# Performance work log

Hardware: AMD Instinct MI355X
Metric: run time of the kernel (lower is better)

Reference implementation:

```python
import jax, jax.numpy as jnp
import numpy as np

B, TZ, TU = 32, 16, 128
E, H, V = 512, 1024, 32000
FREQ_THRES = 4   # cfg.freq_thres: zero out copy prob for most-frequent tokens
LN_EPS = 1e-3


def setup_inputs() -> dict:
    key = jax.random.key(0)
    ks = jax.random.split(key, 16)
    s = lambda k, shape, sc=0.02: jax.random.normal(k, shape, jnp.float32) * sc
    return dict(
        z_enc_out=jax.random.normal(ks[0], (TZ, B, H), jnp.float32),
        pz_proba=jax.nn.softmax(jax.random.normal(ks[1], (TZ, B, V), jnp.float32), axis=-1),
        u_enc_out=jax.random.normal(ks[2], (TU, B, H), jnp.float32),
        m_t_input=jax.random.randint(ks[3], (1, B), 0, V),
        last_hidden=jax.random.normal(ks[4], (1, B, H), jnp.float32),
        emb=s(ks[5], (V, E), 1.0 / np.sqrt(E)),
        Wa_z=s(ks[6], (2 * H, H)), ba_z=jnp.zeros((H,), jnp.float32), v_z=s(ks[7], (H,), 1.0 / np.sqrt(H)),
        Wa_u=s(ks[8], (2 * H, H)), ba_u=jnp.zeros((H,), jnp.float32), v_u=s(ks[9], (H,), 1.0 / np.sqrt(H)),
        W_ih=s(ks[10], (3 * H, E + 2 * H)), W_hh=s(ks[11], (3 * H, H)),
        b_ih=jnp.zeros((3 * H,), jnp.float32), b_hh=jnp.zeros((3 * H,), jnp.float32),
        ln_a=jnp.ones((H,), jnp.float32), ln_b=jnp.zeros((H,), jnp.float32),
        W_proj=s(ks[12], (H, V)), b_proj=jnp.zeros((V,), jnp.float32),
        W_c=s(ks[13], (2 * H, H)), b_c=jnp.zeros((H,), jnp.float32),
        W_v1=s(ks[14], (H, 1)), b_v1=jnp.zeros((1,), jnp.float32),
    )


def _attn(hidden, enc, Wa, ba, v):
    # hidden [1,B,H], enc [T,B,H] -> context [1,B,H]
    hh = jnp.broadcast_to(hidden, enc.shape)                       # [T,B,H]
    energy = jnp.tanh(jnp.concatenate([hh, enc], -1) @ Wa + ba)    # [T,B,H]
    scores = jnp.einsum('tbh,h->bt', energy, v)                    # [B,T]
    w = jax.nn.softmax(scores, axis=1)
    return jnp.einsum('bt,tbh->bh', w, enc)[None]                  # [1,B,H]


def _layernorm(x, a, b):
    mu = jnp.mean(x, axis=-1, keepdims=True)
    sigma = jnp.std(x, axis=-1, keepdims=True, ddof=1)  # torch.std is unbiased
    return (x - mu) / (sigma + LN_EPS) * a + b


def reference(z_enc_out, pz_proba, u_enc_out, m_t_input, last_hidden,
              emb, Wa_z, ba_z, v_z, Wa_u, ba_u, v_u,
              W_ih, W_hh, b_ih, b_hh, ln_a, ln_b,
              W_proj, b_proj, W_c, b_c, W_v1, b_v1):
    m_embed = emb[m_t_input]                                       # [1,B,E]
    z_ctx = _attn(last_hidden, z_enc_out, Wa_z, ba_z, v_z)         # [1,B,H]
    u_ctx = _attn(last_hidden, u_enc_out, Wa_u, ba_u, v_u)         # [1,B,H]
    x = jnp.concatenate([z_ctx, u_ctx, m_embed], -1)[0]            # [B,2H+E]
    h = last_hidden[0]                                             # [B,H]
    # single-step GRU (torch gate order: r, z, n)
    gi = x @ W_ih.T + b_ih
    gh = h @ W_hh.T + b_hh
    ir, iz, inn = jnp.split(gi, 3, axis=-1)
    hr, hz, hn = jnp.split(gh, 3, axis=-1)
    r = jax.nn.sigmoid(ir + hr)
    zg = jax.nn.sigmoid(iz + hz)
    n = jnp.tanh(inn + r * hn)
    h_new = (1.0 - zg) * n + zg * h                                # [B,H]
    gru_out = _layernorm(h_new, ln_a, ln_b)                        # [B,H]
    gen_score = gru_out @ W_proj + b_proj                          # [B,V]
    # tanh-linear copy score over z positions
    g_rep = jnp.broadcast_to(gru_out[None], z_enc_out.shape)       # [Tz,B,H]
    zc = jnp.tanh(jnp.concatenate([z_enc_out, g_rep], -1) @ W_c + b_c)  # [Tz,B,H]
    zc = (zc @ W_v1 + b_v1)[..., 0].T                              # [B,Tz]
    # joint softmax over [gen | copy]
    scores = jax.nn.softmax(jnp.concatenate([gen_score, zc], axis=1), axis=1)
    gen_p, copy_p = scores[:, :V], scores[:, V:]
    copy_v = jnp.einsum('bt,tbv->bv', copy_p, pz_proba)            # mask_prob bmm
    freq_mask = (jnp.arange(V) >= FREQ_THRES).astype(gen_p.dtype)
    proba = gen_p + copy_v * freq_mask
    return proba, h_new[None]
```

## Files before the change

kernel.cpp:

```cpp
#include <hip/hip_runtime.h>
#include <stdint.h>

#define B_ 32
#define TZ_ 16
#define TU_ 128
#define E_ 512
#define H_ 1024
#define V_ 32000
#define X_ 2560
#define H3_ 3072
#define LN_EPS_ 0.001f

typedef unsigned short ushort_t;
typedef ushort_t us4 __attribute__((ext_vector_type(4)));
typedef ushort_t us8 __attribute__((ext_vector_type(8)));
typedef short bf16x8 __attribute__((ext_vector_type(8)));
typedef float f32x4 __attribute__((ext_vector_type(4)));

__device__ __forceinline__ float bf2f(ushort_t u){
  union { unsigned int i; float f; } x; x.i = ((unsigned int)u) << 16; return x.f;
}
__device__ __forceinline__ ushort_t f2b(float f){
  union { float f; unsigned int i; } u; u.f = f;
  unsigned int x = u.i;
  return (ushort_t)((x + 0x7fffu + ((x >> 16) & 1u)) >> 16);
}
__device__ __forceinline__ bool is_bf(const void* lnA){
  return *(const unsigned int*)lnA == 0x3F803F80u;
}
__device__ __forceinline__ float ldg_(const void* p, size_t i, bool isb){
  return isb ? bf2f(((const ushort_t*)p)[i]) : ((const float*)p)[i];
}
__device__ __forceinline__ float sigm(float x){ return 1.0f/(1.0f + __expf(-x)); }
__device__ __forceinline__ float tanh_f(float x){
  float cx = fminf(fmaxf(x, -9.0f), 9.0f);
  float t = __expf(2.0f*cx);
  return (t - 1.0f)/(t + 1.0f);
}

__global__ void k0_init(const void* lh, const void* emb, const int* mt,
                        const void* ba_z, const void* ba_u, const void* b_c,
                        const void* b_ih, const void* b_hh, const void* bpj,
                        const void* lnA,
                        ushort_t* hb, ushort_t* xb, float* hWaZ, float* hWaU,
                        float* sz, float* su, float* gruWc, float* gi, float* gh,
                        float* genscore){
  bool isb = is_bf(lnA);
  int i = blockIdx.x*256 + threadIdx.x;
  if (i < 32768){ hb[i] = f2b(ldg_(lh, i, isb)); return; }
  i -= 32768;
  if (i < 16384){ int b = i >> 9, e = i & 511;
    xb[b*X_ + 2048 + e] = f2b(ldg_(emb, (size_t)(unsigned)mt[b]*E_ + e, isb)); return; }
  i -= 16384;
  if (i < 32768){ hWaZ[i] = ldg_(ba_z, i & 1023, isb); return; }
  i -= 32768;
  if (i < 32768){ hWaU[i] = ldg_(ba_u, i & 1023, isb); return; }
  i -= 32768;
  if (i < 4608){ if (i < 512) sz[i] = 0.f; else su[i-512] = 0.f; return; }
  i -= 4608;
  if (i < 32768){ gruWc[i] = ldg_(b_c, i & 1023, isb); return; }
  i -= 32768;
  if (i < 98304){ gi[i] = ldg_(b_ih, i % H3_, isb); return; }
  i -= 98304;
  if (i < 98304){ gh[i] = ldg_(b_hh, i % H3_, isb); return; }
  i -= 98304;
  if (i < 1024000){
    int b = i / V_;
    int v = i - b*V_;
    genscore[(size_t)b*V_ + v] = ldg_(bpj, v, isb);
  }
}

__global__ void kC_cvt(const void* uenc, const void* zenc, const void* Wih, const void* Whh,
                       const void* lnA,
                       ushort_t* uB, ushort_t* zB, ushort_t* WihB, ushort_t* WhhB){
  bool isb = is_bf(lnA);
  long long i = (long long)(blockIdx.x*256 + threadIdx.x) * 8;
  const long long NU = (long long)TU_*B_*H_;
  const long long NZ = (long long)TZ_*B_*H_;
  const long long NI = (long long)H3_*X_;
  const long long NH = (long long)H3_*H_;
  const void* src; ushort_t* dst;
  if (i < NU){ src = uenc; dst = uB; }
  else if ((i -= NU) < NZ){ src = zenc; dst = zB; }
  else if ((i -= NZ) < NI){ src = Wih; dst = WihB; }
  else if ((i -= NI) < NH){ src = Whh; dst = WhhB; }
  else return;
  if (isb){
    *(us8*)&dst[i] = *(const us8*)((const ushort_t*)src + i);
  } else {
    const float* s = (const float*)src + i;
    float4 a0 = *(const float4*)s, a1 = *(const float4*)(s + 4);
    us8 o;
    o[0]=f2b(a0.x); o[1]=f2b(a0.y); o[2]=f2b(a0.z); o[3]=f2b(a0.w);
    o[4]=f2b(a1.x); o[5]=f2b(a1.y); o[6]=f2b(a1.z); o[7]=f2b(a1.w);
    *(us8*)&dst[i] = o;
  }
}

__global__ void kT_transpose(const void* Wz, const void* Wu, const void* Wc, const void* lnA,
                             ushort_t* tZ, ushort_t* tU, ushort_t* tC,
                             ushort_t* tZt, ushort_t* tUt, ushort_t* tCb){
  bool isb = is_bf(lnA);
  int w = blockIdx.z;
  const void* src = (w==0||w==3)? Wz : (w==1||w==4)? Wu : Wc;
  size_t base = (w==0||w==1||w==5) ? (size_t)H_*H_ : 0;
  ushort_t* dst = (w==0)? tZ : (w==1)? tU : (w==2)? tC : (w==3)? tZt : (w==4)? tUt : tCb;
  __shared__ ushort_t T[64][68];
  int k0 = blockIdx.x*64, j0 = blockIdx.y*64;
  int tx = threadIdx.x & 15, ty = threadIdx.x >> 4;
  if (isb){
    const ushort_t* s = (const ushort_t*)src + base;
    #pragma unroll
    for (int rr=0; rr<4; ++rr){
      int row = ty + rr*16;
      *(us4*)&T[row][tx*4] = *(const us4*)&s[(size_t)(k0+row)*H_ + j0 + tx*4];
    }
  } else {
    const float* s = (const float*)src + base;
    #pragma unroll
    for (int rr=0; rr<4; ++rr){
      int row = ty + rr*16;
      #pragma unroll
      for (int c=0;c<4;c++)
        T[row][tx*4+c] = f2b(s[(size_t)(k0+row)*H_ + j0 + tx*4 + c]);
    }
  }
  __syncthreads();
  #pragma unroll
  for (int rr=0; rr<4; ++rr){
    int row = ty + rr*16;
    us4 o;
    o[0]=T[tx*4+0][row]; o[1]=T[tx*4+1][row]; o[2]=T[tx*4+2][row]; o[3]=T[tx*4+3][row];
    *(us4*)&dst[(size_t)(j0+row)*H_ + k0 + tx*4] = o;
  }
}

__global__ __launch_bounds__(256) void kg_mfma(const ushort_t* Ab0, const ushort_t* Ab1,
                                               const ushort_t* W0, const ushort_t* W1,
                                               float* out0, float* out1, int N){
  const ushort_t* Ab = blockIdx.z ? Ab1 : Ab0;
  const ushort_t* WT = blockIdx.z ? W1 : W0;
  float* out = blockIdx.z ? out1 : out0;
  int j0 = blockIdx.x*128;
  int kchunk = H_ / gridDim.y;
  int kb = blockIdx.y*kchunk;
  __shared__ ushort_t Bs[128*32];
  int tid = threadIdx.x, wid = tid >> 6, lane = tid & 63;
  int q = lane >> 4, n = lane & 15;
  int rrow = tid >> 2, t4 = tid & 3;
  f32x4 acc[2][2];
  #pragma unroll
  for (int r=0;r<2;r++)
    #pragma unroll
    for (int c=0;c<2;c++)
      #pragma unroll
      for (int e=0;e<4;e++) acc[r][c][e] = 0.f;

  for (int kt = 0; kt < kchunk; kt += 32){
    int k = kb + kt;
    __syncthreads();
    #pragma unroll
    for (int p=0;p<2;p++){
      const ushort_t* srcB = WT + (size_t)(j0 + p*64 + rrow)*H_ + k + t4*8;
      __builtin_amdgcn_global_load_lds(srcB, &Bs[(p*64 + wid*16)*32], 16, 0, 0);
    }
    __syncthreads();
    bf16x8 af[2], bfr[2];
    #pragma unroll
    for (int r=0;r<2;r++) af[r] = *(const bf16x8*)&Ab[(size_t)(r*16 + n)*H_ + k + q*8];
    #pragma unroll
    for (int c=0;c<2;c++) bfr[c] = *(const bf16x8*)&Bs[(wid*32 + c*16 + n)*32 + q*8];
    #pragma unroll
    for (int r=0;r<2;r++)
      #pragma unroll
      for (int c=0;c<2;c++)
        acc[r][c] = __builtin_amdgcn_mfma_f32_16x16x32_bf16(af[r], bfr[c], acc[r][c], 0, 0, 0);
  }
  #pragma unroll
  for (int r=0;r<2;r++)
    #pragma unroll
    for (int c=0;c<2;c++)
      #pragma unroll
      for (int i=0;i<4;i++){
        int b = r*16 + q*4 + i;
        int j = j0 + wid*32 + c*16 + n;
        unsafeAtomicAdd(&out[(size_t)b*N + j], acc[r][c][i]);
      }
}

__global__ __launch_bounds__(256) void k2_mfma(const ushort_t* Ab, const ushort_t* WB,
                                               float* out, int K, int kchunk){
  int j0 = blockIdx.x*128;
  int kb = blockIdx.y*kchunk;
  __shared__ ushort_t Bs[128*32];
  int tid = threadIdx.x, wid = tid >> 6, lane = tid & 63;
  int q = lane >> 4, n = lane & 15;
  int rrow = tid >> 2, t4 = tid & 3;
  f32x4 acc[2][2];
  #pragma unroll
  for (int r=0;r<2;r++)
    #pragma unroll
    for (int c=0;c<2;c++)
      #pragma unroll
      for (int e=0;e<4;e++) acc[r][c][e] = 0.f;

  for (int kt = 0; kt < kchunk; kt += 32){
    int k = kb + kt;
    __syncthreads();
    #pragma unroll
    for (int p=0;p<2;p++){
      const ushort_t* srcB = WB + (size_t)(j0 + p*64 + rrow)*K + k + t4*8;
      __builtin_amdgcn_global_load_lds(srcB, &Bs[(p*64 + wid*16)*32], 16, 0, 0);
    }
    __syncthreads();
    bf16x8 af[2], bfr[2];
    #pragma unroll
    for (int r=0;r<2;r++) af[r] = *(const bf16x8*)&Ab[(size_t)(r*16 + n)*K + k + q*8];
    #pragma unroll
    for (int c=0;c<2;c++) bfr[c] = *(const bf16x8*)&Bs[(wid*32 + c*16 + n)*32 + q*8];
    #pragma unroll
    for (int r=0;r<2;r++)
      #pragma unroll
      for (int c=0;c<2;c++)
        acc[r][c] = __builtin_amdgcn_mfma_f32_16x16x32_bf16(af[r], bfr[c], acc[r][c], 0, 0, 0);
  }
  #pragma unroll
  for (int r=0;r<2;r++)
    #pragma unroll
    for (int c=0;c<2;c++)
      #pragma unroll
      for (int i=0;i<4;i++){
        int b = r*16 + q*4 + i;
        int j = j0 + wid*32 + c*16 + n;
        unsafeAtomicAdd(&out[(size_t)b*H3_ + j], acc[r][c][i]);
      }
}

__global__ __launch_bounds__(256) void k6p_mfma(const ushort_t* grub, const void* Wp,
                                                const void* lnA, float* genscore){
  bool isb = is_bf(lnA);
  int j0 = blockIdx.x*128;
  int kb = blockIdx.y*256;
  __shared__ float Ts[32][129];
  int tid = threadIdx.x, wid = tid >> 6, lane = tid & 63;
  int q = lane >> 4, n = lane & 15;
  int lrow = tid >> 3, lcol = (tid & 7)*16;
  f32x4 acc[2][2];
  #pragma unroll
  for (int r=0;r<2;r++)
    #pragma unroll
    for (int c=0;c<2;c++)
      #pragma unroll
      for (int e=0;e<4;e++) acc[r][c][e] = 0.f;

  for (int kt = 0; kt < 256; kt += 32){
    int k = kb + kt;
    __syncthreads();
    if (isb){
      const ushort_t* s = (const ushort_t*)Wp + (size_t)(k + lrow)*V_ + j0 + lcol;
      us8 a0 = *(const us8*)s;
      us8 a1 = *(const us8*)(s + 8);
      #pragma unroll
      for (int e=0;e<8;e++){ Ts[lrow][lcol+e] = bf2f(a0[e]); Ts[lrow][lcol+8+e] = bf2f(a1[e]); }
    } else {
      const float* s = (const float*)Wp + (size_t)(k + lrow)*V_ + j0 + lcol;
      float4 f0 = *(const float4*)s,     f1 = *(const float4*)(s+4);
      float4 f2 = *(const float4*)(s+8), f3 = *(const float4*)(s+12);
      *(float4*)&Ts[lrow][lcol]    = f0;
      *(float4*)&Ts[lrow][lcol+4]  = f1;
      *(float4*)&Ts[lrow][lcol+8]  = f2;
      *(float4*)&Ts[lrow][lcol+12] = f3;
    }
    __syncthreads();
    bf16x8 af[2], bfr[2];
    #pragma unroll
    for (int r=0;r<2;r++) af[r] = *(const bf16x8*)&grub[(size_t)(r*16 + n)*H_ + k + q*8];
    #pragma unroll
    for (int c=0;c<2;c++){
      int vl = wid*32 + c*16 + n;
      us8 o;
      #pragma unroll
      for (int e=0;e<8;e++) o[e] = f2b(Ts[q*8 + e][vl]);
      bfr[c] = *(bf16x8*)&o;
    }
    #pragma unroll
    for (int r=0;r<2;r++)
      #pragma unroll
      for (int c=0;c<2;c++)
        acc[r][c] = __builtin_amdgcn_mfma_f32_16x16x32_bf16(af[r], bfr[c], acc[r][c], 0, 0, 0);
  }
  #pragma unroll
  for (int r=0;r<2;r++)
    #pragma unroll
    for (int c=0;c<2;c++)
      #pragma unroll
      for (int i=0;i<4;i++){
        int b = r*16 + q*4 + i;
        int v = j0 + wid*32 + c*16 + n;
        unsafeAtomicAdd(&genscore[(size_t)b*V_ + v], acc[r][c][i]);
      }
}

__global__ __launch_bounds__(256) void k3_mfma(
    const ushort_t* uB, const ushort_t* zB,
    const ushort_t* tU, const ushort_t* tZ, const ushort_t* tC,
    const float* hWaU, const float* hWaZ,
    const void* v_u, const void* v_z, const void* lnA,
    float* su, float* sz, float* zcpre)
{
  bool isb = is_bf(lnA);
  int which = blockIdx.z;
  int bx = blockIdx.x, nt = blockIdx.y;
  int mt;
  const ushort_t* A; const ushort_t* BT;
  if (which == 0){ A = uB; BT = tU; mt = bx; }
  else {
    int lo = (which==1) ? 8 : 12;
    if (bx < lo || bx >= lo+4) return;
    mt = bx - lo;
    A = zB; BT = (which==1) ? tZ : tC;
  }
  __shared__ ushort_t As[128*32];
  __shared__ ushort_t Bs[64*32];
  int tid = threadIdx.x;
  int wid = tid >> 6, lane = tid & 63;
  int q = lane >> 4, n = lane & 15;
  int wm = wid & 1, wn = wid >> 1;
  int r0 = mt*128, j0 = nt*64;
  f32x4 acc[4][2];
  #pragma unroll
  for (int a=0;a<4;a++)
    #pragma unroll
    for (int c=0;c<2;c++)
      #pragma unroll
      for (int e=0;e<4;e++) acc[a][c][e] = 0.f;

  int rrow = tid >> 2, t4 = tid & 3;

  for (int kt = 0; kt < 32; ++kt){
    __syncthreads();
    #pragma unroll
    for (int p=0;p<2;p++){
      const ushort_t* srcA = A + (size_t)(r0 + p*64 + rrow)*H_ + kt*32 + t4*8;
      __builtin_amdgcn_global_load_lds(srcA, &As[(p*64 + wid*16)*32], 16, 0, 0);
    }
    {
      const ushort_t* srcB = BT + (size_t)(j0 + rrow)*H_ + kt*32 + t4*8;
      __builtin_amdgcn_global_load_lds(srcB, &Bs[(wid*16)*32], 16, 0, 0);
    }
    __syncthreads();
    bf16x8 af[4], bfr[2];
    #pragma unroll
    for (int f=0;f<4;f++) af[f] = *(const bf16x8*)&As[(wm*64 + f*16 + n)*32 + q*8];
    #pragma unroll
    for (int f=0;f<2;f++) bfr[f] = *(const bf16x8*)&Bs[(wn*32 + f*16 + n)*32 + q*8];
    #pragma unroll
    for (int fr=0;fr<4;fr++)
      #pragma unroll
      for (int fn=0;fn<2;fn++)
        acc[fr][fn] = __builtin_amdgcn_mfma_f32_16x16x32_bf16(af[fr], bfr[fn], acc[fr][fn], 0, 0, 0);
  }

  if (which < 2){
    const float* pre = (which==0) ? hWaU : hWaZ;
    const void* vv = (which==0) ? v_u : v_z;
    float* score = (which==0) ? su : sz;
    float s[4][4];
    #pragma unroll
    for (int fr=0;fr<4;fr++)
      #pragma unroll
      for (int i=0;i<4;i++) s[fr][i]=0.f;
    #pragma unroll
    for (int fr=0;fr<4;fr++){
      #pragma unroll
      for (int fn=0;fn<2;fn++){
        int j  = j0 + wn*32 + fn*16 + n;
        float vj = ldg_(vv, j, isb);
        #pragma unroll
        for (int i=0;i<4;i++){
          int rl = wm*64 + fr*16 + q*4 + i;
          int b  = rl & 31;
          s[fr][i] += tanh_f(acc[fr][fn][i] + pre[b*H_ + j]) * vj;
        }
      }
    }
    #pragma unroll
    for (int fr=0;fr<4;fr++)
      #pragma unroll
      for (int i=0;i<4;i++){
        float t = s[fr][i];
        t += __shfl_xor(t, 1);
        t += __shfl_xor(t, 2);
        t += __shfl_xor(t, 4);
        t += __shfl_xor(t, 8);
        if (n == 0){
          int rl = wm*64 + fr*16 + q*4 + i;
          unsafeAtomicAdd(&score[r0 + rl], t);
        }
      }
  } else {
    #pragma unroll
    for (int fr=0;fr<4;fr++)
      #pragma unroll
      for (int fn=0;fn<2;fn++)
        #pragma unroll
        for (int i=0;i<4;i++){
          int rl = wm*64 + fr*16 + q*4 + i;
          int jl = wn*32 + fn*16 + n;
          zcpre[(size_t)(r0 + rl)*H_ + j0 + jl] = acc[fr][fn][i];
        }
  }
}

__global__ void k4_ctx(const float* sz, const float* su,
                       const void* zenc, const void* uenc, const void* lnA, ushort_t* xb){
  bool isb = is_bf(lnA);
  int jc = blockIdx.x, b = blockIdx.y, which = blockIdx.z;
  int T = which ? TU_ : TZ_;
  const float* sc = which ? su : sz;
  const void* enc = which ? uenc : zenc;
  __shared__ float red[256];
  __shared__ float w[TU_];
  int tid = threadIdx.x;
  float v = (tid < T) ? sc[tid*B_ + b] : -1e30f;
  red[tid] = v; __syncthreads();
  for (int s=128; s>0; s>>=1){ if (tid < s) red[tid] = fmaxf(red[tid], red[tid+s]); __syncthreads(); }
  float m = red[0]; __syncthreads();
  float e = (tid < T) ? __expf(v - m) : 0.f;
  red[tid] = e; __syncthreads();
  for (int s=128; s>0; s>>=1){ if (tid < s) red[tid] += red[tid+s]; __syncthreads(); }
  float S = red[0]; __syncthreads();
  if (tid < T) w[tid] = e / S;
  __syncthreads();
  int j = jc*256 + tid;
  float acc = 0.f;
  #pragma unroll 4
  for (int t=0; t<T; ++t) acc = fmaf(w[t], ldg_(enc, (size_t)(t*B_ + b)*H_ + j, isb), acc);
  xb[b*X_ + which*H_ + j] = f2b(acc);
}

__global__ __launch_bounds__(1024) void k5_gru(const float* gi, const float* gh,
                       const void* lh, const void* ln_a, const void* ln_b,
                       ushort_t* grub, float* hout){
  bool isb = is_bf(ln_a);
  int b = blockIdx.x, tid = threadIdx.x;
  __shared__ float red[1024];
  int j = tid;
  float ir = gi[(size_t)b*H3_ + j], iz = gi[(size_t)b*H3_ + 1024 + j], inn = gi[(size_t)b*H3_ + 2048 + j];
  float hr = gh[(size_t)b*H3_ + j], hz = gh[(size_t)b*H3_ + 1024 + j], hn = gh[(size_t)b*H3_ + 2048 + j];
  float hv = ldg_(lh, b*H_ + j, isb);
  float r  = sigm(ir + hr);
  float zg = sigm(iz + hz);
  float nn = tanh_f(inn + r*hn);
  float h2 = (1.f - zg)*nn + zg*hv;
  hout[b*H_ + j] = h2;
  red[tid] = h2; __syncthreads();
  for (int s=512;s>0;s>>=1){ if(tid<s) red[tid]+=red[tid+s]; __syncthreads(); }
  float mu = red[0] / 1024.f; __syncthreads();
  red[tid] = h2*h2; __syncthreads();
  for (int s=512;s>0;s>>=1){ if(tid<s) red[tid]+=red[tid+s]; __syncthreads(); }
  float var = (red[0] - 1024.f*mu*mu) / 1023.f;
  float sg = sqrtf(fmaxf(var, 0.f));
  float inv = 1.f/(sg + LN_EPS_);
  float g = (h2 - mu)*inv*ldg_(ln_a, j, isb) + ldg_(ln_b, j, isb);
  grub[b*H_ + j] = f2b(g);
}

__global__ void k7_zc(const float* zcpre, const float* gruWc, const void* Wv1,
                      const void* b_v1, const void* lnA, float* zc){
  bool isb = is_bf(lnA);
  int r = blockIdx.x, b = r & 31, tid = threadIdx.x;
  __shared__ float red[256];
  float s = 0.f;
  #pragma unroll
  for (int jj=0;jj<4;jj++){
    int j = tid + jj*256;
    float e = tanh_f(zcpre[(size_t)r*H_ + j] + gruWc[b*H_ + j]);
    s = fmaf(e, ldg_(Wv1, j, isb), s);
  }
  red[tid] = s; __syncthreads();
  for (int st=128;st>0;st>>=1){ if(tid<st) red[tid]+=red[tid+st]; __syncthreads(); }
  if (tid==0) zc[r] = red[0] + ldg_(b_v1, 0, isb);
}

__global__ void k8a(const float* genscore, float* statpart){
  int v = blockIdx.x*256 + threadIdx.x;
  int b = blockIdx.y, tid = threadIdx.x;
  __shared__ float red[256];
  float g = genscore[(size_t)b*V_ + v];
  red[tid] = g; __syncthreads();
  for (int s=128;s>0;s>>=1){ if(tid<s) red[tid]=fmaxf(red[tid],red[tid+s]); __syncthreads(); }
  float m = red[0]; __syncthreads();
  float e = __expf(g - m);
  red[tid] = e; __syncthreads();
  for (int s=128;s>0;s>>=1){ if(tid<s) red[tid]+=red[tid+s]; __syncthreads(); }
  if (tid==0){ statpart[(b*125 + blockIdx.x)*2] = m; statpart[(b*125 + blockIdx.x)*2+1] = red[0]; }
}

__global__ void k8b(const float* statpart, const float* zc, float* stats, float* copyp){
  int b = blockIdx.x, tid = threadIdx.x;
  __shared__ float red[128];
  float m = -1e30f, s = 0.f;
  if (tid < 125){ m = statpart[(b*125 + tid)*2]; s = statpart[(b*125 + tid)*2 + 1]; }
  float zv = (tid < 16) ? zc[tid*B_ + b] : -1e30f;
  red[tid] = fmaxf(m, zv); __syncthreads();
  for (int st=64;st>0;st>>=1){ if(tid<st) red[tid]=fmaxf(red[tid],red[tid+st]); __syncthreads(); }
  float M = red[0]; __syncthreads();
  float zp = (tid < 125) ? s*__expf(m - M) : 0.f;
  if (tid < 16) zp += __expf(zv - M);
  red[tid] = zp; __syncthreads();
  for (int st=64;st>0;st>>=1){ if(tid<st) red[tid]+=red[tid+st]; __syncthreads(); }
  float invZ = 1.f/red[0];
  if (tid < 16) copyp[b*16 + tid] = __expf(zv - M)*invZ;
  if (tid == 0){ stats[b*2] = M; stats[b*2+1] = invZ; }
}

__global__ void k8c(const float* genscore, const float* stats, const float* copyp,
                    const void* pz, const void* lnA, float* out){
  bool isb = is_bf(lnA);
  int v = blockIdx.x*256 + threadIdx.x;
  int b = blockIdx.y;
  float M = stats[b*2], invZ = stats[b*2+1];
  float p = __expf(genscore[(size_t)b*V_ + v] - M)*invZ;
  if (v >= 4){
    float cv = 0.f;
    if (isb){
      const ushort_t* pzp = (const ushort_t*)pz;
      #pragma unroll
      for (int t=0;t<16;t++)
        cv = fmaf(copyp[b*16 + t], bf2f(pzp[(size_t)(t*B_ + b)*V_ + v]), cv);
    } else {
      const float* pzp = (const float*)pz;
      #pragma unroll
      for (int t=0;t<16;t++)
        cv = fmaf(copyp[b*16 + t], pzp[(size_t)(t*B_ + b)*V_ + v], cv);
    }
    p += cv;
  }
  out[(size_t)b*V_ + v] = p;
}

extern "C" void kernel_launch(void* const* d_in, const int* in_sizes, int n_in,
                              void* d_out, int out_size, void* d_ws, size_t ws_size,
                              hipStream_t stream){
  const void* z_enc = d_in[0];
  const void* pz    = d_in[1];
  const void* u_enc = d_in[2];
  const int*  m_t   = (const int*)d_in[3];
  const void* lh    = d_in[4];
  const void* emb   = d_in[5];
  const void* Wa_z  = d_in[6];
  const void* ba_z  = d_in[7];
  const void* v_z   = d_in[8];
  const void* Wa_u  = d_in[9];
  const void* ba_u  = d_in[10];
  const void* v_u   = d_in[11];
  const void* W_ih  = d_in[12];
  const void* W_hh  = d_in[13];
  const void* b_ih  = d_in[14];
  const void* b_hh  = d_in[15];
  const void* ln_a  = d_in[16];
  const void* ln_b  = d_in[17];
  const void* W_proj= d_in[18];
  const void* b_proj= d_in[19];
  const void* W_c   = d_in[20];
  const void* b_c   = d_in[21];
  const void* W_v1  = d_in[22];
  const void* b_v1  = d_in[23];

  float* wsf = (float*)d_ws;
  size_t o = 0;
  auto alloc = [&](size_t n){ float* p = wsf + o; o += n; return p; };
  float* hWaZ  = alloc(B_*H_);
  float* hWaU  = alloc(B_*H_);
  float* sz    = alloc(TZ_*B_);
  float* su    = alloc(TU_*B_);
  float* gruWc = alloc(B_*H_);
  float* zcpre = alloc((size_t)TZ_*B_*H_);
  float* zcv   = alloc(TZ_*B_);
  float* gi    = alloc((size_t)B_*H3_);
  float* gh    = alloc((size_t)B_*H3_);
  float* genscore = alloc((size_t)B_*V_);
  float* statpart = alloc(B_*125*2);
  float* stats = alloc(B_*2);
  float* copyp = alloc(B_*TZ_);
  o = (o + 7) & ~(size_t)7;
  ushort_t* wT = (ushort_t*)(wsf + o);
  ushort_t* tZ  = wT;
  ushort_t* tU  = wT + (size_t)H_*H_;
  ushort_t* tC  = wT + (size_t)2*H_*H_;
  ushort_t* tZt = wT + (size_t)3*H_*H_;
  ushort_t* tUt = wT + (size_t)4*H_*H_;
  ushort_t* tCb = wT + (size_t)5*H_*H_;
  o += (size_t)6*H_*H_/2;
  ushort_t* uB = (ushort_t*)(wsf + o);
  o += (size_t)TU_*B_*H_/2;
  ushort_t* zB = (ushort_t*)(wsf + o);
  o += (size_t)TZ_*B_*H_/2;
  ushort_t* WihB = (ushort_t*)(wsf + o);
  o += (size_t)H3_*X_/2;
  ushort_t* WhhB = (ushort_t*)(wsf + o);
  o += (size_t)H3_*H_/2;
  ushort_t* xb = (ushort_t*)(wsf + o);
  o += (size_t)B_*X_/2;
  ushort_t* hb = (ushort_t*)(wsf + o);
  o += (size_t)B_*H_/2;
  ushort_t* grub = (ushort_t*)(wsf + o);
  o += (size_t)B_*H_/2;
  float* outp = (float*)d_out;
  float* hout = outp + (size_t)B_*V_;

  k0_init<<<5362, 256, 0, stream>>>(lh, emb, m_t, ba_z, ba_u, b_c, b_ih, b_hh, b_proj, ln_a,
                                    hb, xb, hWaZ, hWaU, sz, su, gruWc, gi, gh, genscore);
  kC_cvt<<<7680, 256, 0, stream>>>(u_enc, z_enc, W_ih, W_hh, ln_a, uB, zB, WihB, WhhB);
  kT_transpose<<<dim3(16,16,6), 256, 0, stream>>>(Wa_z, Wa_u, W_c, ln_a, tZ, tU, tC, tZt, tUt, tCb);
  kg_mfma<<<dim3(8,8,2), 256, 0, stream>>>(hb, hb, tZt, tUt, hWaZ, hWaU, H_);
  k2_mfma<<<dim3(24,16), 256, 0, stream>>>(hb, WhhB, gh, H_, 64);
  k3_mfma<<<dim3(32,16,3), 256, 0, stream>>>(uB, zB, tU, tZ, tC, hWaU, hWaZ, v_u, v_z, ln_a, su, sz, zcpre);
  k4_ctx<<<dim3(4,32,2), 256, 0, stream>>>(sz, su, z_enc, u_enc, ln_a, xb);
  k2_mfma<<<dim3(24,20), 256, 0, stream>>>(xb, WihB, gi, X_, 128);
  k5_gru<<<32, 1024, 0, stream>>>(gi, gh, lh, ln_a, ln_b, grub, hout);
  kg_mfma<<<dim3(8,8,1), 256, 0, stream>>>(grub, grub, tCb, tCb, gruWc, gruWc, H_);
  k7_zc<<<512, 256, 0, stream>>>(zcpre, gruWc, W_v1, b_v1, ln_a, zcv);
  k6p_mfma<<<dim3(250,4), 256, 0, stream>>>(grub, W_proj, ln_a, genscore);
  k8a<<<dim3(125,32), 256, 0, stream>>>(genscore, statpart);
  k8b<<<32, 128, 0, stream>>>(statpart, zcv, stats, copyp);
  k8c<<<dim3(125,32), 256, 0, stream>>>(genscore, stats, copyp, pz, ln_a, outp);
}
```

Before: 460.9 us.

## Fuse prep kernels, split-K attention GEMM with separate score kernel

Merges the init, conversion and transpose kernels into one launch that also zeroes the new split-K accumulators. The attention energy GEMM is now split along K into two slices that accumulate atomically into fp32 buffers, and a separate kernel applies tanh and the v projection to produce the scores. The vocab projection also gets twice the K-split. The aim is more blocks in flight and fewer launches. In exchange it writes and re-reads large fp32 energy tensors, needs extra zeroing, and issues more atomics.

```diff
diff --git a/kernel.cpp b/kernel.cpp
--- a/kernel.cpp
+++ b/kernel.cpp
@@ -38,101 +38,114 @@
   return (t - 1.0f)/(t + 1.0f);
 }
 
-__global__ void k0_init(const void* lh, const void* emb, const int* mt,
-                        const void* ba_z, const void* ba_u, const void* b_c,
-                        const void* b_ih, const void* b_hh, const void* bpj,
-                        const void* lnA,
-                        ushort_t* hb, ushort_t* xb, float* hWaZ, float* hWaU,
-                        float* sz, float* su, float* gruWc, float* gi, float* gh,
-                        float* genscore){
+#define PB0 5344
+#define PB1 13024
+#define PB2 14560
+#define PB3 19680
+__global__ void kprep(const void* lh, const void* emb, const int* mt,
+                      const void* ba_z, const void* ba_u, const void* b_c,
+                      const void* b_ih, const void* b_hh, const void* bpj,
+                      const void* uenc, const void* zenc, const void* Wih, const void* Whh,
+                      const void* Wz, const void* Wu, const void* Wc,
+                      const void* lnA,
+                      ushort_t* hb, ushort_t* xb, float* hWaZ, float* hWaU,
+                      float* gruWc, float* gi, float* gh, float* genscore,
+                      ushort_t* uB, ushort_t* zB, ushort_t* WihB, ushort_t* WhhB,
+                      ushort_t* tZ, ushort_t* tU, ushort_t* tC,
+                      ushort_t* tZt, ushort_t* tUt, ushort_t* tCb,
+                      float* zeroBase){
+  __shared__ ushort_t T[64][68];
   bool isb = is_bf(lnA);
-  int i = blockIdx.x*256 + threadIdx.x;
-  if (i < 32768){ hb[i] = f2b(ldg_(lh, i, isb)); return; }
-  i -= 32768;
-  if (i < 16384){ int b = i >> 9, e = i & 511;
-    xb[b*X_ + 2048 + e] = f2b(ldg_(emb, (size_t)(unsigned)mt[b]*E_ + e, isb)); return; }
-  i -= 16384;
-  if (i < 32768){ hWaZ[i] = ldg_(ba_z, i & 1023, isb); return; }
-  i -= 32768;
-  if (i < 32768){ hWaU[i] = ldg_(ba_u, i & 1023, isb); return; }
-  i -= 32768;
-  if (i < 4608){ if (i < 512) sz[i] = 0.f; else su[i-512] = 0.f; return; }
-  i -= 4608;
-  if (i < 32768){ gruWc[i] = ldg_(b_c, i & 1023, isb); return; }
-  i -= 32768;
-  if (i < 98304){ gi[i] = ldg_(b_ih, i % H3_, isb); return; }
-  i -= 98304;
-  if (i < 98304){ gh[i] = ldg_(b_hh, i % H3_, isb); return; }
-  i -= 98304;
-  if (i < 1024000){
-    int b = i / V_;
-    int v = i - b*V_;
-    genscore[(size_t)b*V_ + v] = ldg_(bpj, v, isb);
-  }
-}
-
-__global__ void kC_cvt(const void* uenc, const void* zenc, const void* Wih, const void* Whh,
-                       const void* lnA,
-                       ushort_t* uB, ushort_t* zB, ushort_t* WihB, ushort_t* WhhB){
-  bool isb = is_bf(lnA);
-  long long i = (long long)(blockIdx.x*256 + threadIdx.x) * 8;
-  const long long NU = (long long)TU_*B_*H_;
-  const long long NZ = (long long)TZ_*B_*H_;
-  const long long NI = (long long)H3_*X_;
-  const long long NH = (long long)H3_*H_;
-  const void* src; ushort_t* dst;
-  if (i < NU){ src = uenc; dst = uB; }
-  else if ((i -= NU) < NZ){ src = zenc; dst = zB; }
-  else if ((i -= NZ) < NI){ src = Wih; dst = WihB; }
-  else if ((i -= NI) < NH){ src = Whh; dst = WhhB; }
-  else return;
-  if (isb){
-    *(us8*)&dst[i] = *(const us8*)((const ushort_t*)src + i);
-  } else {
-    const float* s = (const float*)src + i;
-    float4 a0 = *(const float4*)s, a1 = *(const float4*)(s + 4);
-    us8 o;
-    o[0]=f2b(a0.x); o[1]=f2b(a0.y); o[2]=f2b(a0.z); o[3]=f2b(a0.w);
-    o[4]=f2b(a1.x); o[5]=f2b(a1.y); o[6]=f2b(a1.z); o[7]=f2b(a1.w);
-    *(us8*)&dst[i] = o;
-  }
-}
-
-__global__ void kT_transpose(const void* Wz, const void* Wu, const void* Wc, const void* lnA,
-                             ushort_t* tZ, ushort_t* tU, ushort_t* tC,
-                             ushort_t* tZt, ushort_t* tUt, ushort_t* tCb){
-  bool isb = is_bf(lnA);
-  int w = blockIdx.z;
-  const void* src = (w==0||w==3)? Wz : (w==1||w==4)? Wu : Wc;
-  size_t base = (w==0||w==1||w==5) ? (size_t)H_*H_ : 0;
-  ushort_t* dst = (w==0)? tZ : (w==1)? tU : (w==2)? tC : (w==3)? tZt : (w==4)? tUt : tCb;
-  __shared__ ushort_t T[64][68];
-  int k0 = blockIdx.x*64, j0 = blockIdx.y*64;
-  int tx = threadIdx.x & 15, ty = threadIdx.x >> 4;
-  if (isb){
-    const ushort_t* s = (const ushort_t*)src + base;
+  int bid = blockIdx.x, tid = threadIdx.x;
+  if (bid < PB0){
+    int i = bid*256 + tid;
+    if (i < 32768){ hb[i] = f2b(ldg_(lh, i, isb)); return; }
+    i -= 32768;
+    if (i < 16384){ int b = i >> 9, e = i & 511;
+      xb[b*X_ + 2048 + e] = f2b(ldg_(emb, (size_t)(unsigned)mt[b]*E_ + e, isb)); return; }
+    i -= 16384;
+    if (i < 32768){ hWaZ[i] = ldg_(ba_z, i & 1023, isb); return; }
+    i -= 32768;
+    if (i < 32768){ hWaU[i] = ldg_(ba_u, i & 1023, isb); return; }
+    i -= 32768;
+    if (i < 32768){ gruWc[i] = ldg_(b_c, i & 1023, isb); return; }
+    i -= 32768;
+    if (i < 98304){ gi[i] = ldg_(b_ih, i % H3_, isb); return; }
+    i -= 98304;
+    if (i < 98304){ gh[i] = ldg_(b_hh, i % H3_, isb); return; }
+    i -= 98304;
+    if (i < 1024000){
+      int b = i / V_;
+      int v = i - b*V_;
+      genscore[(size_t)b*V_ + v] = ldg_(bpj, v, isb);
+    }
+    return;
+  }
+  if (bid < PB1){
+    long long i = (long long)((bid - PB0)*256 + tid) * 8;
+    const long long NU = (long long)TU_*B_*H_;
+    const long long NZ = (long long)TZ_*B_*H_;
+    const long long NI = (long long)H3_*X_;
+    const long long NH = (long long)H3_*H_;
+    const void* src; ushort_t* dst;
+    if (i < NU){ src = uenc; dst = uB; }
+    else if ((i -= NU) < NZ){ src = zenc; dst = zB; }
+    else if ((i -= NZ) < NI){ src = Wih; dst = WihB; }
+    else if ((i -= NI) < NH){ src = Whh; dst = WhhB; }
+    else return;
+    if (isb){
+      *(us8*)&dst[i] = *(const us8*)((const ushort_t*)src + i);
+    } else {
+      const float* s = (const float*)src + i;
+      float4 a0 = *(const float4*)s, a1 = *(const float4*)(s + 4);
+      us8 o;
+      o[0]=f2b(a0.x); o[1]=f2b(a0.y); o[2]=f2b(a0.z); o[3]=f2b(a0.w);
+      o[4]=f2b(a1.x); o[5]=f2b(a1.y); o[6]=f2b(a1.z); o[7]=f2b(a1.w);
+      *(us8*)&dst[i] = o;
+    }
+    return;
+  }
+  if (bid < PB2){
+    int idx = bid - PB1;
+    int w = idx >> 8;
+    int rem = idx & 255;
+    int bx = rem & 15, by = rem >> 4;
+    const void* src = (w==0||w==3)? Wz : (w==1||w==4)? Wu : Wc;
+    size_t base = (w==0||w==1||w==5) ? (size_t)H_*H_ : 0;
+    ushort_t* dst = (w==0)? tZ : (w==1)? tU : (w==2)? tC : (w==3)? tZt : (w==4)? tUt : tCb;
+    int k0 = bx*64, j0 = by*64;
+    int tx = tid & 15, ty = tid >> 4;
+    if (isb){
+      const ushort_t* s = (const ushort_t*)src + base;
+      #pragma unroll
+      for (int rr=0; rr<4; ++rr){
+        int row = ty + rr*16;
+        *(us4*)&T[row][tx*4] = *(const us4*)&s[(size_t)(k0+row)*H_ + j0 + tx*4];
+      }
+    } else {
+      const float* s = (const float*)src + base;
+      #pragma unroll
+      for (int rr=0; rr<4; ++rr){
+        int row = ty + rr*16;
+        #pragma unroll
+        for (int c=0;c<4;c++)
+          T[row][tx*4+c] = f2b(s[(size_t)(k0+row)*H_ + j0 + tx*4 + c]);
+      }
+    }
+    __syncthreads();
     #pragma unroll
     for (int rr=0; rr<4; ++rr){
       int row = ty + rr*16;
-      *(us4*)&T[row][tx*4] = *(const us4*)&s[(size_t)(k0+row)*H_ + j0 + tx*4];
-    }
-  } else {
-    const float* s = (const float*)src + base;
-    #pragma unroll
-    for (int rr=0; rr<4; ++rr){
-      int row = ty + rr*16;
-      #pragma unroll
-      for (int c=0;c<4;c++)
-        T[row][tx*4+c] = f2b(s[(size_t)(k0+row)*H_ + j0 + tx*4 + c]);
-    }
-  }
-  __syncthreads();
-  #pragma unroll
-  for (int rr=0; rr<4; ++rr){
-    int row = ty + rr*16;
-    us4 o;
-    o[0]=T[tx*4+0][row]; o[1]=T[tx*4+1][row]; o[2]=T[tx*4+2][row]; o[3]=T[tx*4+3][row];
-    *(us4*)&dst[(size_t)(j0+row)*H_ + k0 + tx*4] = o;
+      us4 o;
+      o[0]=T[tx*4+0][row]; o[1]=T[tx*4+1][row]; o[2]=T[tx*4+2][row]; o[3]=T[tx*4+3][row];
+      *(us4*)&dst[(size_t)(j0+row)*H_ + k0 + tx*4] = o;
+    }
+    return;
+  }
+  if (bid < PB3){
+    int i = (bid - PB2)*256 + tid;
+    float4 z = {0.f,0.f,0.f,0.f};
+    *(float4*)&zeroBase[(size_t)i*4] = z;
   }
 }
 
@@ -237,11 +250,100 @@
       }
 }
 
+__global__ __launch_bounds__(256) void kg3_mfma(
+    const ushort_t* uB, const ushort_t* zB,
+    const ushort_t* tU, const ushort_t* tZ, const ushort_t* tC,
+    float* E_u, float* E_z, float* E_c)
+{
+  int bx = blockIdx.x, nt = blockIdx.y, ks = blockIdx.z;
+  int mt;
+  const ushort_t* A; const ushort_t* BT; float* E;
+  if (bx < 32){ A = uB; BT = tU; E = E_u; mt = bx; }
+  else if (bx < 36){ A = zB; BT = tZ; E = E_z; mt = bx - 32; }
+  else { A = zB; BT = tC; E = E_c; mt = bx - 36; }
+  __shared__ ushort_t As[128*32];
+  __shared__ ushort_t Bs[64*32];
+  int tid = threadIdx.x;
+  int wid = tid >> 6, lane = tid & 63;
+  int q = lane >> 4, n = lane & 15;
+  int wm = wid & 1, wn = wid >> 1;
+  int r0 = mt*128, j0 = nt*64;
+  int kbase = ks*512;
+  f32x4 acc[4][2];
+  #pragma unroll
+  for (int a=0;a<4;a++)
+    #pragma unroll
+    for (int c=0;c<2;c++)
+      #pragma unroll
+      for (int e=0;e<4;e++) acc[a][c][e] = 0.f;
+
+  int rrow = tid >> 2, t4 = tid & 3;
+
+  for (int kt = 0; kt < 16; ++kt){
+    int k = kbase + kt*32;
+    __syncthreads();
+    #pragma unroll
+    for (int p=0;p<2;p++){
+      const ushort_t* srcA = A + (size_t)(r0 + p*64 + rrow)*H_ + k + t4*8;
+      __builtin_amdgcn_global_load_lds(srcA, &As[(p*64 + wid*16)*32], 16, 0, 0);
+    }
+    {
+      const ushort_t* srcB = BT + (size_t)(j0 + rrow)*H_ + k + t4*8;
+      __builtin_amdgcn_global_load_lds(srcB, &Bs[(wid*16)*32], 16, 0, 0);
+    }
+    __syncthreads();
+    bf16x8 af[4], bfr[2];
+    #pragma unroll
+    for (int f=0;f<4;f++) af[f] = *(const bf16x8*)&As[(wm*64 + f*16 + n)*32 + q*8];
+    #pragma unroll
+    for (int f=0;f<2;f++) bfr[f] = *(const bf16x8*)&Bs[(wn*32 + f*16 + n)*32 + q*8];
+    #pragma unroll
+    for (int fr=0;fr<4;fr++)
+      #pragma unroll
+      for (int fn=0;fn<2;fn++)
+        acc[fr][fn] = __builtin_amdgcn_mfma_f32_16x16x32_bf16(af[fr], bfr[fn], acc[fr][fn], 0, 0, 0);
+  }
+
+  #pragma unroll
+  for (int fr=0;fr<4;fr++)
+    #pragma unroll
+    for (int fn=0;fn<2;fn++)
+      #pragma unroll
+      for (int i=0;i<4;i++){
+        int rl = wm*64 + fr*16 + q*4 + i;
+        int jl = wn*32 + fn*16 + n;
+        unsafeAtomicAdd(&E[(size_t)(r0 + rl)*H_ + j0 + jl], acc[fr][fn][i]);
+      }
+}
+
+__global__ void kE_score(const float* E_u, const float* E_z,
+                         const float* hWaU, const float* hWaZ,
+                         const void* v_u, const void* v_z, const void* lnA,
+                         float* su, float* sz){
+  bool isb = is_bf(lnA);
+  int r = blockIdx.x, tid = threadIdx.x;
+  const float* E; const float* pre; const void* vv; float* sc; int rr;
+  if (r < 4096){ E = E_u; pre = hWaU; vv = v_u; sc = su; rr = r; }
+  else { E = E_z; pre = hWaZ; vv = v_z; sc = sz; rr = r - 4096; }
+  int b = rr & 31;
+  __shared__ float red[256];
+  float s = 0.f;
+  #pragma unroll
+  for (int jj=0;jj<4;jj++){
+    int j = tid + jj*256;
+    s = fmaf(tanh_f(E[(size_t)rr*H_ + j] + pre[b*H_ + j]), ldg_(vv, j, isb), s);
+  }
+  red[tid] = s; __syncthreads();
+  for (int st=128;st>0;st>>=1){ if(tid<st) red[tid]+=red[tid+st]; __syncthreads(); }
+  if (tid==0) sc[rr] = red[0];
+}
+
 __global__ __launch_bounds__(256) void k6p_mfma(const ushort_t* grub, const void* Wp,
                                                 const void* lnA, float* genscore){
   bool isb = is_bf(lnA);
   int j0 = blockIdx.x*128;
-  int kb = blockIdx.y*256;
+  int kchunk = H_ / gridDim.y;
+  int kb = blockIdx.y*kchunk;
   __shared__ float Ts[32][129];
   int tid = threadIdx.x, wid = tid >> 6, lane = tid & 63;
   int q = lane >> 4, n = lane & 15;
@@ -254,7 +356,7 @@
       #pragma unroll
       for (int e=0;e<4;e++) acc[r][c][e] = 0.f;
 
-  for (int kt = 0; kt < 256; kt += 32){
+  for (int kt = 0; kt < kchunk; kt += 32){
     int k = kb + kt;
     __syncthreads();
     if (isb){
@@ -300,117 +402,6 @@
         int v = j0 + wid*32 + c*16 + n;
         unsafeAtomicAdd(&genscore[(size_t)b*V_ + v], acc[r][c][i]);
       }
-}
-
-__global__ __launch_bounds__(256) void k3_mfma(
-    const ushort_t* uB, const ushort_t* zB,
-    const ushort_t* tU, const ushort_t* tZ, const ushort_t* tC,
-    const float* hWaU, const float* hWaZ,
-    const void* v_u, const void* v_z, const void* lnA,
-    float* su, float* sz, float* zcpre)
-{
-  bool isb = is_bf(lnA);
-  int which = blockIdx.z;
-  int bx = blockIdx.x, nt = blockIdx.y;
-  int mt;
-  const ushort_t* A; const ushort_t* BT;
-  if (which == 0){ A = uB; BT = tU; mt = bx; }
-  else {
-    int lo = (which==1) ? 8 : 12;
-    if (bx < lo || bx >= lo+4) return;
-    mt = bx - lo;
-    A = zB; BT = (which==1) ? tZ : tC;
-  }
-  __shared__ ushort_t As[128*32];
-  __shared__ ushort_t Bs[64*32];
-  int tid = threadIdx.x;
-  int wid = tid >> 6, lane = tid & 63;
-  int q = lane >> 4, n = lane & 15;
-  int wm = wid & 1, wn = wid >> 1;
-  int r0 = mt*128, j0 = nt*64;
-  f32x4 acc[4][2];
-  #pragma unroll
-  for (int a=0;a<4;a++)
-    #pragma unroll
-    for (int c=0;c<2;c++)
-      #pragma unroll
-      for (int e=0;e<4;e++) acc[a][c][e] = 0.f;
-
-  int rrow = tid >> 2, t4 = tid & 3;
-
-  for (int kt = 0; kt < 32; ++kt){
-    __syncthreads();
-    #pragma unroll
-    for (int p=0;p<2;p++){
-      const ushort_t* srcA = A + (size_t)(r0 + p*64 + rrow)*H_ + kt*32 + t4*8;
-      __builtin_amdgcn_global_load_lds(srcA, &As[(p*64 + wid*16)*32], 16, 0, 0);
-    }
-    {
-      const ushort_t* srcB = BT + (size_t)(j0 + rrow)*H_ + kt*32 + t4*8;
-      __builtin_amdgcn_global_load_lds(srcB, &Bs[(wid*16)*32], 16, 0, 0);
-    }
-    __syncthreads();
-    bf16x8 af[4], bfr[2];
-    #pragma unroll
-    for (int f=0;f<4;f++) af[f] = *(const bf16x8*)&As[(wm*64 + f*16 + n)*32 + q*8];
-    #pragma unroll
-    for (int f=0;f<2;f++) bfr[f] = *(const bf16x8*)&Bs[(wn*32 + f*16 + n)*32 + q*8];
-    #pragma unroll
-    for (int fr=0;fr<4;fr++)
-      #pragma unroll
-      for (int fn=0;fn<2;fn++)
-        acc[fr][fn] = __builtin_amdgcn_mfma_f32_16x16x32_bf16(af[fr], bfr[fn], acc[fr][fn], 0, 0, 0);
-  }
-
-  if (which < 2){
-    const float* pre = (which==0) ? hWaU : hWaZ;
-    const void* vv = (which==0) ? v_u : v_z;
-    float* score = (which==0) ? su : sz;
-    float s[4][4];
-    #pragma unroll
-    for (int fr=0;fr<4;fr++)
-      #pragma unroll
-      for (int i=0;i<4;i++) s[fr][i]=0.f;
-    #pragma unroll
-    for (int fr=0;fr<4;fr++){
-      #pragma unroll
-      for (int fn=0;fn<2;fn++){
-        int j  = j0 + wn*32 + fn*16 + n;
-        float vj = ldg_(vv, j, isb);
-        #pragma unroll
-        for (int i=0;i<4;i++){
-          int rl = wm*64 + fr*16 + q*4 + i;
-          int b  = rl & 31;
-          s[fr][i] += tanh_f(acc[fr][fn][i] + pre[b*H_ + j]) * vj;
-        }
-      }
-    }
-    #pragma unroll
-    for (int fr=0;fr<4;fr++)
-      #pragma unroll
-      for (int i=0;i<4;i++){
-        float t = s[fr][i];
-        t += __shfl_xor(t, 1);
-        t += __shfl_xor(t, 2);
-        t += __shfl_xor(t, 4);
-        t += __shfl_xor(t, 8);
-        if (n == 0){
-          int rl = wm*64 + fr*16 + q*4 + i;
-          unsafeAtomicAdd(&score[r0 + rl], t);
-        }
-      }
-  } else {
-    #pragma unroll
-    for (int fr=0;fr<4;fr++)
-      #pragma unroll
-      for (int fn=0;fn<2;fn++)
-        #pragma unroll
-        for (int i=0;i<4;i++){
-          int rl = wm*64 + fr*16 + q*4 + i;
-          int jl = wn*32 + fn*16 + n;
-          zcpre[(size_t)(r0 + rl)*H_ + j0 + jl] = acc[fr][fn][i];
-        }
-  }
 }
 
 __global__ void k4_ctx(const float* sz, const float* su,
@@ -578,6 +569,8 @@
   float* su    = alloc(TU_*B_);
   float* gruWc = alloc(B_*H_);
   float* zcpre = alloc((size_t)TZ_*B_*H_);
+  float* E_u   = alloc((size_t)TU_*B_*H_);
+  float* E_z   = alloc((size_t)TZ_*B_*H_);
   float* zcv   = alloc(TZ_*B_);
   float* gi    = alloc((size_t)B_*H3_);
   float* gh    = alloc((size_t)B_*H3_);
@@ -611,19 +604,21 @@
   float* outp = (float*)d_out;
   float* hout = outp + (size_t)B_*V_;
 
-  k0_init<<<5362, 256, 0, stream>>>(lh, emb, m_t, ba_z, ba_u, b_c, b_ih, b_hh, b_proj, ln_a,
-                                    hb, xb, hWaZ, hWaU, sz, su, gruWc, gi, gh, genscore);
-  kC_cvt<<<7680, 256, 0, stream>>>(u_enc, z_enc, W_ih, W_hh, ln_a, uB, zB, WihB, WhhB);
-  kT_transpose<<<dim3(16,16,6), 256, 0, stream>>>(Wa_z, Wa_u, W_c, ln_a, tZ, tU, tC, tZt, tUt, tCb);
+  kprep<<<PB3, 256, 0, stream>>>(lh, emb, m_t, ba_z, ba_u, b_c, b_ih, b_hh, b_proj,
+                                 u_enc, z_enc, W_ih, W_hh, Wa_z, Wa_u, W_c, ln_a,
+                                 hb, xb, hWaZ, hWaU, gruWc, gi, gh, genscore,
+                                 uB, zB, WihB, WhhB, tZ, tU, tC, tZt, tUt, tCb,
+                                 zcpre );
   kg_mfma<<<dim3(8,8,2), 256, 0, stream>>>(hb, hb, tZt, tUt, hWaZ, hWaU, H_);
   k2_mfma<<<dim3(24,16), 256, 0, stream>>>(hb, WhhB, gh, H_, 64);
-  k3_mfma<<<dim3(32,16,3), 256, 0, stream>>>(uB, zB, tU, tZ, tC, hWaU, hWaZ, v_u, v_z, ln_a, su, sz, zcpre);
+  kg3_mfma<<<dim3(40,16,2), 256, 0, stream>>>(uB, zB, tU, tZ, tC, E_u, E_z, zcpre);
+  kE_score<<<4608, 256, 0, stream>>>(E_u, E_z, hWaU, hWaZ, v_u, v_z, ln_a, su, sz);
   k4_ctx<<<dim3(4,32,2), 256, 0, stream>>>(sz, su, z_enc, u_enc, ln_a, xb);
   k2_mfma<<<dim3(24,20), 256, 0, stream>>>(xb, WihB, gi, X_, 128);
   k5_gru<<<32, 1024, 0, stream>>>(gi, gh, lh, ln_a, ln_b, grub, hout);
   kg_mfma<<<dim3(8,8,1), 256, 0, stream>>>(grub, grub, tCb, tCb, gruWc, gruWc, H_);
   k7_zc<<<512, 256, 0, stream>>>(zcpre, gruWc, W_v1, b_v1, ln_a, zcv);
-  k6p_mfma<<<dim3(250,4), 256, 0, stream>>>(grub, W_proj, ln_a, genscore);
+  k6p_mfma<<<dim3(250,8), 256, 0, stream>>>(grub, W_proj, ln_a, genscore);
   k8a<<<dim3(125,32), 256, 0, stream>>>(genscore, statpart);
   k8b<<<32, 128, 0, stream>>>(statpart, zcv, stats, copyp);
   k8c<<<dim3(125,32), 256, 0, stream>>>(genscore, stats, copyp, pz, ln_a, outp);
```

Result: slower. 491.9 us (+6.7%).
